# Optimization experiments

Hardware: AMD Instinct MI355X
Metric: run time of the kernel (lower is better)

## Reference

```python
import jax, jax.numpy as jnp
import numpy as np

N = 100000   # nodes
E = 1000000  # edges
F = 128      # num_features
H = 64       # hidden_size
C = 1        # num_classes
G = 128      # num graphs in batch


def gcn_conv(x, W, b, src, dst, deg_inv_sqrt):
    # PyG GCNConv: add self-loops, symmetric normalization D^-1/2 (A+I) D^-1/2, then X W + b
    h = x @ W                                   # [N, H]
    norm = deg_inv_sqrt[src] * deg_inv_sqrt[dst]  # [E]
    msg = h[src] * norm[:, None]                # gather + scale, [E, H]
    out = jnp.zeros_like(h).at[dst].add(msg)    # scatter-add to targets
    out = out + h * (deg_inv_sqrt ** 2)[:, None]  # self-loop contribution
    return out + b


def setup_inputs() -> dict:
    key = jax.random.key(0)
    ks = jax.random.split(key, 12)
    x = jax.random.normal(ks[0], (N, F), dtype=jnp.float32)
    edge_index = jax.random.randint(ks[1], (2, E), 0, N, dtype=jnp.int32).astype(jnp.int64)
    batch = jnp.sort(jax.random.randint(ks[2], (N,), 0, G, dtype=jnp.int32)).astype(jnp.int64)
    def glorot(k, fan_in, fan_out):
        s = np.float32(np.sqrt(6.0 / (fan_in + fan_out)))
        return jax.random.uniform(k, (fan_in, fan_out), jnp.float32, -s, s)
    return {
        "x": x, "edge_index": edge_index, "batch": batch,
        "W1": glorot(ks[3], F, H), "b1": jnp.zeros((H,), jnp.float32),
        "W2": glorot(ks[4], H, H), "b2": jnp.zeros((H,), jnp.float32),
        "Wl1": glorot(ks[5], H, H), "bl1": jnp.zeros((H,), jnp.float32),
        "Wl2": glorot(ks[6], H, C), "bl2": jnp.zeros((C,), jnp.float32),
    }


def reference(x, edge_index, batch, W1, b1, W2, b2, Wl1, bl1, Wl2, bl2):
    src, dst = edge_index[0], edge_index[1]
    # degree with self-loops: 1 + in-degree(target)
    deg = jnp.ones((N,), x.dtype).at[dst].add(jnp.ones((E,), x.dtype))
    deg_inv_sqrt = jax.lax.rsqrt(deg)
    h = jax.nn.relu(gcn_conv(x, W1, b1, src, dst, deg_inv_sqrt))
    h = jax.nn.relu(gcn_conv(h, W2, b2, src, dst, deg_inv_sqrt))
    g = jax.ops.segment_sum(h, batch, num_segments=G)  # global_add_pool, [G, H]
    g = jax.nn.relu(g @ Wl1 + bl1)
    out = g @ Wl2 + bl2                                # [G, 1]
    return out.squeeze(axis=1)                         # [G]
```

## Files before the change

### kernel.cpp

```cpp
#include <hip/hip_runtime.h>

#define NN 100000
#define EE 1000000
#define FF 128
#define HH 64
#define GG 128
#define NB 391
#define MMB 1563

__global__ void k_hist(const int* __restrict__ ei, int* __restrict__ cnt) {
    int e = blockIdx.x * 256 + threadIdx.x;
    if (e < EE) atomicAdd(&cnt[ei[EE + e]], 1);
}

__global__ void k_scan1(const int* __restrict__ cnt, int* __restrict__ part,
                        float* __restrict__ dis) {
    int i = blockIdx.x * 256 + threadIdx.x;
    int c = (i < NN) ? cnt[i] : 0;
    if (i < NN) dis[i] = rsqrtf((float)(c + 1));
    int v = (i < NN) ? c : 0;
    for (int o = 1; o < 64; o <<= 1) v += __shfl_xor(v, o);
    __shared__ int ws[4];
    if ((threadIdx.x & 63) == 0) ws[threadIdx.x >> 6] = v;
    __syncthreads();
    if (threadIdx.x == 0) part[blockIdx.x] = ws[0] + ws[1] + ws[2] + ws[3];
}

__global__ void k_scan2(int* __restrict__ part) {
    __shared__ int buf[512];
    int t = threadIdx.x;
    int v = (t < NB) ? part[t] : 0;
    buf[t] = v; __syncthreads();
    for (int o = 1; o < 512; o <<= 1) {
        int u = (t >= o) ? buf[t - o] : 0;
        __syncthreads();
        buf[t] += u;
        __syncthreads();
    }
    if (t < NB) part[t] = buf[t] - v;
}

__global__ void k_scan3(const int* __restrict__ cnt, const int* __restrict__ part,
                        int* __restrict__ row_ptr, int* __restrict__ cursor) {
    int i = blockIdx.x * 256 + threadIdx.x;
    int v = (i < NN) ? cnt[i] : 0;
    int lane = threadIdx.x & 63, w = threadIdx.x >> 6;
    int incl = v;
    for (int o = 1; o < 64; o <<= 1) { int u = __shfl_up(incl, o); if (lane >= o) incl += u; }
    __shared__ int ws[4];
    if (lane == 63) ws[w] = incl;
    __syncthreads();
    int woff = 0;
    for (int k = 0; k < w; ++k) woff += ws[k];
    int excl = incl - v + woff + part[blockIdx.x];
    if (i < NN) {
        row_ptr[i] = excl;
        cursor[i]  = excl;
    }
    if (i == 0) row_ptr[NN] = EE;
}

template<int K>
__device__ __forceinline__ void
mm_body(const float* __restrict__ X, const float* __restrict__ W,
        const float* __restrict__ dis, unsigned* __restrict__ Y8,
        float* __restrict__ S, float* __restrict__ Wl, int bid) {
    for (int i = threadIdx.x; i < K * HH; i += 256) Wl[i] = W[i];
    __syncthreads();
    const int lane = threadIdx.x & 63;
    const int wv   = threadIdx.x >> 6;
    const int c4   = (lane & 15) * 4;
    const int rsg  = lane >> 4;
    const int r0   = bid * 64 + wv * 16 + rsg * 4;

    const float* xr0; const float* xr1; const float* xr2; const float* xr3;
    {
        int a = r0,     b_ = r0 + 1, c = r0 + 2, d = r0 + 3;
        if (a > NN - 1) a = NN - 1;
        if (b_ > NN - 1) b_ = NN - 1;
        if (c > NN - 1) c = NN - 1;
        if (d > NN - 1) d = NN - 1;
        xr0 = X + (size_t)a * K; xr1 = X + (size_t)b_ * K;
        xr2 = X + (size_t)c * K; xr3 = X + (size_t)d * K;
    }
    float4 acc0 = {0,0,0,0}, acc1 = {0,0,0,0}, acc2 = {0,0,0,0}, acc3 = {0,0,0,0};

#pragma unroll 8
    for (int k4 = 0; k4 < K / 4; ++k4) {
        const float4 x0 = *(const float4*)(xr0 + k4 * 4);
        const float4 x1 = *(const float4*)(xr1 + k4 * 4);
        const float4 x2 = *(const float4*)(xr2 + k4 * 4);
        const float4 x3 = *(const float4*)(xr3 + k4 * 4);
        const float4 w0 = *(const float4*)&Wl[(k4 * 4 + 0) * HH + c4];
        const float4 w1 = *(const float4*)&Wl[(k4 * 4 + 1) * HH + c4];
        const float4 w2 = *(const float4*)&Wl[(k4 * 4 + 2) * HH + c4];
        const float4 w3 = *(const float4*)&Wl[(k4 * 4 + 3) * HH + c4];
#define FMA4(A, XS) \
        A.x = fmaf(XS.x, w0.x, A.x); A.y = fmaf(XS.x, w0.y, A.y); \
        A.z = fmaf(XS.x, w0.z, A.z); A.w = fmaf(XS.x, w0.w, A.w); \
        A.x = fmaf(XS.y, w1.x, A.x); A.y = fmaf(XS.y, w1.y, A.y); \
        A.z = fmaf(XS.y, w1.z, A.z); A.w = fmaf(XS.y, w1.w, A.w); \
        A.x = fmaf(XS.z, w2.x, A.x); A.y = fmaf(XS.z, w2.y, A.y); \
        A.z = fmaf(XS.z, w2.z, A.z); A.w = fmaf(XS.z, w2.w, A.w); \
        A.x = fmaf(XS.w, w3.x, A.x); A.y = fmaf(XS.w, w3.y, A.y); \
        A.z = fmaf(XS.w, w3.z, A.z); A.w = fmaf(XS.w, w3.w, A.w);
        FMA4(acc0, x0) FMA4(acc1, x1) FMA4(acc2, x2) FMA4(acc3, x3)
#undef FMA4
    }
#define STORE(I, A) { \
        const int r = r0 + I; \
        if (r < NN) { \
            const float d = dis[r]; \
            const float ax = A.x * d, ay = A.y * d, az = A.z * d, aw = A.w * d; \
            float m = fmaxf(fmaxf(fabsf(ax), fabsf(ay)), fmaxf(fabsf(az), fabsf(aw))); \
            m = fmaxf(m, __shfl_xor(m, 1)); m = fmaxf(m, __shfl_xor(m, 2)); \
            m = fmaxf(m, __shfl_xor(m, 4)); m = fmaxf(m, __shfl_xor(m, 8)); \
            const float inv = 127.0f / m; \
            int q0 = __float2int_rn(ax * inv), q1 = __float2int_rn(ay * inv); \
            int q2 = __float2int_rn(az * inv), q3 = __float2int_rn(aw * inv); \
            if (m == 0.0f) { q0 = q1 = q2 = q3 = 0; } \
            const unsigned pk = (q0 & 0xff) | ((q1 & 0xff) << 8) | \
                                ((q2 & 0xff) << 16) | ((q3 & 0xff) << 24); \
            Y8[(size_t)r * 16 + (c4 >> 2)] = pk; \
            if (c4 == 0) S[r] = m * (1.0f / 127.0f); \
        } }
    STORE(0, acc0) STORE(1, acc1) STORE(2, acc2) STORE(3, acc3)
#undef STORE
}

template<int K>
__global__ __launch_bounds__(256) void
k_matmul_b(const float* __restrict__ X, const float* __restrict__ W,
           const float* __restrict__ dis, unsigned* __restrict__ Y8,
           float* __restrict__ S) {
    __shared__ float Wl[K * HH];
    mm_body<K>(X, W, dis, Y8, S, Wl, blockIdx.x);
}

__global__ __launch_bounds__(256) void
k_mm1_place(const float* __restrict__ X, const float* __restrict__ W,
            const float* __restrict__ dis, unsigned* __restrict__ Y8,
            float* __restrict__ S, const int* __restrict__ ei,
            int* __restrict__ cursor, int* __restrict__ srcs) {
    __shared__ float Wl[FF * HH];
    if (blockIdx.x < MMB) {
        mm_body<FF>(X, W, dis, Y8, S, Wl, blockIdx.x);
    } else {
        int e = (blockIdx.x - MMB) * 256 + threadIdx.x;
        if (e < EE) {
            int d = ei[EE + e];
            int p = atomicAdd(&cursor[d], 1);
            srcs[p] = ei[e];
        }
    }
}

template<bool POOL>
__global__ __launch_bounds__(256) void
k_gconv(const int* __restrict__ row_ptr, const int* __restrict__ srcs,
        const float* __restrict__ dis, const unsigned* __restrict__ H8,
        const float* __restrict__ S, const float* __restrict__ b,
        float* __restrict__ Out, const int* __restrict__ batch,
        float* __restrict__ g) {
    const int node = blockIdx.x * 4 + (threadIdx.x >> 6);
    const int lane = threadIdx.x & 63;
    const int li   = lane & 15;
    const int qr   = lane >> 4;
    const int p0   = row_ptr[node];
    const int deg  = row_ptr[node + 1] - p0;
    const int items  = deg + 1;
    const int nbatch = (items + 7) >> 3;

    float ac0 = 0.f, ac1 = 0.f, ac2 = 0.f, ac3 = 0.f;

#define IDX(bi, dA, dB) { \
        const int iA = 8 * (bi) + qr, iB = iA + 4; \
        dA = srcs[p0 + (iA < deg ? iA : 0)]; \
        dB = srcs[p0 + (iB < deg ? iB : 0)]; }
#define VAL(bi, sA, sB, vA, vB, gA, gB) { \
        const int iA = 8 * (bi) + qr, iB = iA + 4; \
        const int rA = (iA < deg) ? sA : node; \
        const int rB = (iB < deg) ? sB : node; \
        vA = H8[(size_t)rA * 16 + li];  gA = S[rA]; \
        vB = H8[(size_t)rB * 16 + li];  gB = S[rB]; }
#define CONSUME(bi, vA, vB, gA, gB) { \
        const int iA = 8 * (bi) + qr, iB = iA + 4; \
        const float s0 = (iA <= deg) ? gA : 0.f; \
        const float s1 = (iB <= deg) ? gB : 0.f; \
        ac0 = fmaf(s0, (float)(signed char)(vA      ), ac0); \
        ac1 = fmaf(s0, (float)(signed char)(vA >> 8 ), ac1); \
        ac2 = fmaf(s0, (float)(signed char)(vA >> 16), ac2); \
        ac3 = fmaf(s0, (float)(signed char)(vA >> 24), ac3); \
        ac0 = fmaf(s1, (float)(signed char)(vB      ), ac0); \
        ac1 = fmaf(s1, (float)(signed char)(vB >> 8 ), ac1); \
        ac2 = fmaf(s1, (float)(signed char)(vB >> 16), ac2); \
        ac3 = fmaf(s1, (float)(signed char)(vB >> 24), ac3); }

    int sA0, sA1, sB0, sB1;
    unsigned vA0, vA1;
    float gA0, gA1;
    IDX(0, sA0, sA1);
    VAL(0, sA0, sA1, vA0, vA1, gA0, gA1);
    IDX(1, sB0, sB1);
    for (int bi = 1; bi < nbatch; ++bi) {
        unsigned vB0, vB1;
        float gB0, gB1;
        VAL(bi, sB0, sB1, vB0, vB1, gB0, gB1);
        IDX(bi + 1, sB0, sB1);
        CONSUME(bi - 1, vA0, vA1, gA0, gA1);
        vA0 = vB0; vA1 = vB1; gA0 = gB0; gA1 = gB1;
    }
    CONSUME(nbatch - 1, vA0, vA1, gA0, gA1);
#undef IDX
#undef VAL
#undef CONSUME

    ac0 += __shfl_xor(ac0, 16); ac0 += __shfl_xor(ac0, 32);
    ac1 += __shfl_xor(ac1, 16); ac1 += __shfl_xor(ac1, 32);
    ac2 += __shfl_xor(ac2, 16); ac2 += __shfl_xor(ac2, 32);
    ac3 += __shfl_xor(ac3, 16); ac3 += __shfl_xor(ac3, 32);
    const float c0 = __shfl(ac0, lane >> 2);
    const float c1 = __shfl(ac1, lane >> 2);
    const float c2 = __shfl(ac2, lane >> 2);
    const float c3 = __shfl(ac3, lane >> 2);
    const int m = lane & 3;
    float acc = (m == 0) ? c0 : (m == 1) ? c1 : (m == 2) ? c2 : c3;

    const float dd = dis[node];
    float v = acc * dd + b[lane];
    v = fmaxf(v, 0.0f);
    if (POOL) {
        unsafeAtomicAdd(&g[(size_t)batch[node] * HH + lane], v);
    } else {
        Out[(size_t)node * HH + lane] = v;
    }
}

__global__ void k_head1(const float* __restrict__ g, const float* __restrict__ W,
                        const float* __restrict__ b, float* __restrict__ g2) {
    const int idx = blockIdx.x * 256 + threadIdx.x;
    const int row = idx >> 6;
    const int col = idx & 63;
    const float* gr = g + (size_t)row * HH;
    float acc = b[col];
#pragma unroll
    for (int k = 0; k < HH; ++k) acc = fmaf(gr[k], W[k * HH + col], acc);
    g2[idx] = acc > 0.0f ? acc : 0.0f;
}

__global__ void k_head2(const float* __restrict__ g2, const float* __restrict__ W,
                        const float* __restrict__ b, float* __restrict__ out) {
    const int r = threadIdx.x;
    if (r >= GG) return;
    const float* gr = g2 + (size_t)r * HH;
    float acc = 0.0f;
#pragma unroll
    for (int k = 0; k < HH; ++k) acc = fmaf(gr[k], W[k], acc);
    out[r] = acc + b[0];
}

extern "C" void kernel_launch(void* const* d_in, const int* in_sizes, int n_in,
                              void* d_out, int out_size, void* d_ws, size_t ws_size,
                              hipStream_t stream) {
    const float* x   = (const float*)d_in[0];
    const int*   ei  = (const int*)d_in[1];
    const int*   bat = (const int*)d_in[2];
    const float* W1  = (const float*)d_in[3];
    const float* b1  = (const float*)d_in[4];
    const float* W2  = (const float*)d_in[5];
    const float* b2  = (const float*)d_in[6];
    const float* Wl1 = (const float*)d_in[7];
    const float* bl1 = (const float*)d_in[8];
    const float* Wl2 = (const float*)d_in[9];
    const float* bl2 = (const float*)d_in[10];
    float* out = (float*)d_out;

    char* w = (char*)d_ws;
    float*    dis     = (float*)(w);
    int*      cnt     = (int*)  (w + 400128);
    int*      row_ptr = (int*)  (w + 800256);
    int*      cursor  = (int*)  (w + 1200640);
    int*      part    = (int*)  (w + 1600768);
    int*      srcs    = (int*)  (w + 1602816);
    float*    S       = (float*)(w + 5602816);
    unsigned* H8      = (unsigned*)(w + 6002944);
    float*    A       = (float*)(w + 12402944);
    float*    g       = (float*)(w + 38002944);
    float*    g2      = g + GG * HH;

    hipMemsetAsync(cnt, 0, (size_t)NN * sizeof(int), stream);
    k_hist <<<(EE + 255) / 256, 256, 0, stream>>>(ei, cnt);
    k_scan1<<<NB, 256, 0, stream>>>(cnt, part, dis);
    k_scan2<<<1, 512, 0, stream>>>(part);
    k_scan3<<<NB, 256, 0, stream>>>(cnt, part, row_ptr, cursor);

    k_mm1_place<<<MMB + (EE + 255) / 256, 256, 0, stream>>>(x, W1, dis, H8, S, ei, cursor, srcs);
    k_gconv<false><<<NN / 4, 256, 0, stream>>>(row_ptr, srcs, dis, H8, S, b1, A, nullptr, nullptr);

    k_matmul_b<HH><<<(NN + 63) / 64, 256, 0, stream>>>(A, W2, dis, H8, S);
    hipMemsetAsync(g, 0, (size_t)GG * HH * sizeof(float), stream);
    k_gconv<true><<<NN / 4, 256, 0, stream>>>(row_ptr, srcs, dis, H8, S, b2, nullptr, bat, g);

    k_head1<<<(GG * HH) / 256, 256, 0, stream>>>(g, Wl1, bl1, g2);
    k_head2<<<1, 128, 0, stream>>>(g2, Wl2, bl2, out);
}
```

Baseline: 292.4 us.

## Replace gather aggregation with source-side push into per-edge message buffers

```diff
diff --git a/kernel.cpp b/kernel.cpp
--- a/kernel.cpp
+++ b/kernel.cpp
@@ -7,18 +7,36 @@
 #define GG 128
 #define NB 391
 #define MMB 1563
-
-__global__ void k_hist(const int* __restrict__ ei, int* __restrict__ cnt) {
+#define NQ 4
+#define QN 25000
+#define QCAP 260000
+
+__device__ inline unsigned short f2bf(float f) {
+    unsigned u = __float_as_uint(f);
+    u += 0x7fffu + ((u >> 16) & 1u);
+    return (unsigned short)(u >> 16);
+}
+__device__ inline float bf2f(unsigned short h) {
+    return __uint_as_float((unsigned)h << 16);
+}
+
+__global__ void k_hist2(const int* __restrict__ ei, int* __restrict__ cnt,
+                        int* __restrict__ cnt2) {
     int e = blockIdx.x * 256 + threadIdx.x;
-    if (e < EE) atomicAdd(&cnt[ei[EE + e]], 1);
-}
-
-__global__ void k_scan1(const int* __restrict__ cnt, int* __restrict__ part,
-                        float* __restrict__ dis) {
-    int i = blockIdx.x * 256 + threadIdx.x;
-    int c = (i < NN) ? cnt[i] : 0;
-    if (i < NN) dis[i] = rsqrtf((float)(c + 1));
-    int v = (i < NN) ? c : 0;
+    if (e < EE) {
+        atomicAdd(&cnt[ei[EE + e]], 1);
+        atomicAdd(&cnt2[ei[e]], 1);
+    }
+}
+
+__global__ void k_scan1(const int* __restrict__ cnt, const int* __restrict__ cnt2,
+                        int* __restrict__ part, float* __restrict__ dis) {
+    const int half = (blockIdx.x >= NB) ? 1 : 0;
+    const int bid  = blockIdx.x - half * NB;
+    const int i = bid * 256 + threadIdx.x;
+    const int* c = half ? cnt2 : cnt;
+    int v = (i < NN) ? c[i] : 0;
+    if (!half && i < NN) dis[i] = rsqrtf((float)(v + 1));
     for (int o = 1; o < 64; o <<= 1) v += __shfl_xor(v, o);
     __shared__ int ws[4];
     if ((threadIdx.x & 63) == 0) ws[threadIdx.x >> 6] = v;
@@ -27,24 +45,33 @@
 }
 
 __global__ void k_scan2(int* __restrict__ part) {
-    __shared__ int buf[512];
-    int t = threadIdx.x;
-    int v = (t < NB) ? part[t] : 0;
+    __shared__ int buf[1024];
+    const int t = threadIdx.x;
+    const int h = t >> 9;
+    const int j = t & 511;
+    int v = (j < NB) ? part[h * NB + j] : 0;
     buf[t] = v; __syncthreads();
     for (int o = 1; o < 512; o <<= 1) {
-        int u = (t >= o) ? buf[t - o] : 0;
+        int u = (j >= o) ? buf[t - o] : 0;
         __syncthreads();
         buf[t] += u;
         __syncthreads();
     }
-    if (t < NB) part[t] = buf[t] - v;
-}
-
-__global__ void k_scan3(const int* __restrict__ cnt, const int* __restrict__ part,
-                        int* __restrict__ row_ptr, int* __restrict__ cursor) {
-    int i = blockIdx.x * 256 + threadIdx.x;
-    int v = (i < NN) ? cnt[i] : 0;
-    int lane = threadIdx.x & 63, w = threadIdx.x >> 6;
+    if (j < NB) part[h * NB + j] = buf[t] - v;
+}
+
+__global__ void k_scan3(const int* __restrict__ cnt, const int* __restrict__ cnt2,
+                        const int* __restrict__ part,
+                        int* __restrict__ row_ptr, int* __restrict__ row_ptr2,
+                        int* __restrict__ cursor, int* __restrict__ cursor2) {
+    const int half = (blockIdx.x >= NB) ? 1 : 0;
+    const int bid  = blockIdx.x - half * NB;
+    const int i = bid * 256 + threadIdx.x;
+    const int* c  = half ? cnt2 : cnt;
+    int* rp  = half ? row_ptr2 : row_ptr;
+    int* cur = half ? cursor2 : cursor;
+    int v = (i < NN) ? c[i] : 0;
+    const int lane = threadIdx.x & 63, w = threadIdx.x >> 6;
     int incl = v;
     for (int o = 1; o < 64; o <<= 1) { int u = __shfl_up(incl, o); if (lane >= o) incl += u; }
     __shared__ int ws[4];
@@ -52,17 +79,14 @@
     __syncthreads();
     int woff = 0;
     for (int k = 0; k < w; ++k) woff += ws[k];
-    int excl = incl - v + woff + part[blockIdx.x];
-    if (i < NN) {
-        row_ptr[i] = excl;
-        cursor[i]  = excl;
-    }
-    if (i == 0) row_ptr[NN] = EE;
-}
-
-template<int K>
+    const int excl = incl - v + woff + part[blockIdx.x];
+    if (i < NN) { rp[i] = excl; cur[i] = excl; }
+    if (i == 0) rp[NN] = EE;
+}
+
+template<int K, int XBF>
 __device__ __forceinline__ void
-mm_body(const float* __restrict__ X, const float* __restrict__ W,
+mm_body(const void* __restrict__ Xv, const float* __restrict__ W,
         const float* __restrict__ dis, unsigned* __restrict__ Y8,
         float* __restrict__ S, float* __restrict__ Wl, int bid) {
     for (int i = threadIdx.x; i < K * HH; i += 256) Wl[i] = W[i];
@@ -73,24 +97,38 @@
     const int rsg  = lane >> 4;
     const int r0   = bid * 64 + wv * 16 + rsg * 4;
 
-    const float* xr0; const float* xr1; const float* xr2; const float* xr3;
+    const char* Xb = (const char*)Xv;
+    const size_t rb = (size_t)K * (XBF ? 2 : 4);
+    const char* xr0; const char* xr1; const char* xr2; const char* xr3;
     {
-        int a = r0,     b_ = r0 + 1, c = r0 + 2, d = r0 + 3;
+        int a = r0, b_ = r0 + 1, c = r0 + 2, d = r0 + 3;
         if (a > NN - 1) a = NN - 1;
         if (b_ > NN - 1) b_ = NN - 1;
         if (c > NN - 1) c = NN - 1;
         if (d > NN - 1) d = NN - 1;
-        xr0 = X + (size_t)a * K; xr1 = X + (size_t)b_ * K;
-        xr2 = X + (size_t)c * K; xr3 = X + (size_t)d * K;
+        xr0 = Xb + (size_t)a * rb; xr1 = Xb + (size_t)b_ * rb;
+        xr2 = Xb + (size_t)c * rb; xr3 = Xb + (size_t)d * rb;
     }
     float4 acc0 = {0,0,0,0}, acc1 = {0,0,0,0}, acc2 = {0,0,0,0}, acc3 = {0,0,0,0};
 
 #pragma unroll 8
     for (int k4 = 0; k4 < K / 4; ++k4) {
-        const float4 x0 = *(const float4*)(xr0 + k4 * 4);
-        const float4 x1 = *(const float4*)(xr1 + k4 * 4);
-        const float4 x2 = *(const float4*)(xr2 + k4 * 4);
-        const float4 x3 = *(const float4*)(xr3 + k4 * 4);
+        float4 x0, x1, x2, x3;
+        if (XBF) {
+            ushort4 u0 = *(const ushort4*)(xr0 + k4 * 8);
+            ushort4 u1 = *(const ushort4*)(xr1 + k4 * 8);
+            ushort4 u2 = *(const ushort4*)(xr2 + k4 * 8);
+            ushort4 u3 = *(const ushort4*)(xr3 + k4 * 8);
+            x0 = {bf2f(u0.x), bf2f(u0.y), bf2f(u0.z), bf2f(u0.w)};
+            x1 = {bf2f(u1.x), bf2f(u1.y), bf2f(u1.z), bf2f(u1.w)};
+            x2 = {bf2f(u2.x), bf2f(u2.y), bf2f(u2.z), bf2f(u2.w)};
+            x3 = {bf2f(u3.x), bf2f(u3.y), bf2f(u3.z), bf2f(u3.w)};
+        } else {
+            x0 = *(const float4*)(xr0 + k4 * 16);
+            x1 = *(const float4*)(xr1 + k4 * 16);
+            x2 = *(const float4*)(xr2 + k4 * 16);
+            x3 = *(const float4*)(xr3 + k4 * 16);
+        }
         const float4 w0 = *(const float4*)&Wl[(k4 * 4 + 0) * HH + c4];
         const float4 w1 = *(const float4*)&Wl[(k4 * 4 + 1) * HH + c4];
         const float4 w2 = *(const float4*)&Wl[(k4 * 4 + 2) * HH + c4];
@@ -128,93 +166,92 @@
 #undef STORE
 }
 
-template<int K>
+template<int K, int XBF>
 __global__ __launch_bounds__(256) void
-k_matmul_b(const float* __restrict__ X, const float* __restrict__ W,
+k_matmul_b(const void* __restrict__ X, const float* __restrict__ W,
            const float* __restrict__ dis, unsigned* __restrict__ Y8,
            float* __restrict__ S) {
     __shared__ float Wl[K * HH];
-    mm_body<K>(X, W, dis, Y8, S, Wl, blockIdx.x);
+    mm_body<K, XBF>(X, W, dis, Y8, S, Wl, blockIdx.x);
 }
 
 __global__ __launch_bounds__(256) void
 k_mm1_place(const float* __restrict__ X, const float* __restrict__ W,
             const float* __restrict__ dis, unsigned* __restrict__ Y8,
             float* __restrict__ S, const int* __restrict__ ei,
-            int* __restrict__ cursor, int* __restrict__ srcs) {
+            int* __restrict__ cursor, int* __restrict__ cursor2,
+            int* __restrict__ csc_pos) {
     __shared__ float Wl[FF * HH];
     if (blockIdx.x < MMB) {
-        mm_body<FF>(X, W, dis, Y8, S, Wl, blockIdx.x);
+        mm_body<FF, 0>(X, W, dis, Y8, S, Wl, blockIdx.x);
     } else {
         int e = (blockIdx.x - MMB) * 256 + threadIdx.x;
         if (e < EE) {
-            int d = ei[EE + e];
-            int p = atomicAdd(&cursor[d], 1);
-            srcs[p] = ei[e];
+            const int s = ei[e], d = ei[EE + e];
+            const int p = atomicAdd(&cursor[d], 1);
+            const int q = atomicAdd(&cursor2[s], 1);
+            csc_pos[q] = p;
+        }
+    }
+}
+
+__global__ __launch_bounds__(256) void
+k_scatA(const int* __restrict__ row_ptr2, const int* __restrict__ csc_pos,
+        const unsigned* __restrict__ H8, const float* __restrict__ S,
+        const int* __restrict__ row_ptr, int n0, int n1,
+        unsigned* __restrict__ msg, float* __restrict__ msgS) {
+    const int node = blockIdx.x * 16 + (threadIdx.x >> 4);
+    const int li   = threadIdx.x & 15;
+    const int tbase = (threadIdx.x & 63) & ~15;
+    const unsigned rv = H8[(size_t)node * 16 + li];
+    const float sv = S[node];
+    const int q0 = row_ptr2[node], q1 = row_ptr2[node + 1];
+    const int PB0 = row_ptr[n0], PB1 = row_ptr[n1];
+    for (int base = q0; base < q1; base += 16) {
+        const int myp = (base + li < q1) ? csc_pos[base + li] : -1;
+        const int cnt = min(16, q1 - base);
+        for (int j = 0; j < cnt; ++j) {
+            const int p = __shfl(myp, tbase + j);
+            if (p >= PB0 && p < PB1) {
+                msg[(size_t)(p - PB0) * 16 + li] = rv;
+                if (li == 0) msgS[p - PB0] = sv;
+            }
         }
     }
 }
 
 template<bool POOL>
 __global__ __launch_bounds__(256) void
-k_gconv(const int* __restrict__ row_ptr, const int* __restrict__ srcs,
-        const float* __restrict__ dis, const unsigned* __restrict__ H8,
-        const float* __restrict__ S, const float* __restrict__ b,
-        float* __restrict__ Out, const int* __restrict__ batch,
-        float* __restrict__ g) {
-    const int node = blockIdx.x * 4 + (threadIdx.x >> 6);
+k_gconvB(const int* __restrict__ row_ptr, const float* __restrict__ dis,
+         const unsigned* __restrict__ H8, const float* __restrict__ S,
+         const unsigned* __restrict__ msg, const float* __restrict__ msgS,
+         const float* __restrict__ b, int n0,
+         unsigned short* __restrict__ A, const int* __restrict__ batch,
+         float* __restrict__ g) {
+    const int node = n0 + blockIdx.x * 4 + (threadIdx.x >> 6);
     const int lane = threadIdx.x & 63;
-    const int li   = lane & 15;
-    const int qr   = lane >> 4;
-    const int p0   = row_ptr[node];
-    const int deg  = row_ptr[node + 1] - p0;
-    const int items  = deg + 1;
-    const int nbatch = (items + 7) >> 3;
-
+    const int li = lane & 15, qr = lane >> 4;
+    const int PB0 = row_ptr[n0];
+    const int p0  = row_ptr[node] - PB0;
+    const int deg = row_ptr[node + 1] - PB0 - p0;
     float ac0 = 0.f, ac1 = 0.f, ac2 = 0.f, ac3 = 0.f;
-
-#define IDX(bi, dA, dB) { \
-        const int iA = 8 * (bi) + qr, iB = iA + 4; \
-        dA = srcs[p0 + (iA < deg ? iA : 0)]; \
-        dB = srcs[p0 + (iB < deg ? iB : 0)]; }
-#define VAL(bi, sA, sB, vA, vB, gA, gB) { \
-        const int iA = 8 * (bi) + qr, iB = iA + 4; \
-        const int rA = (iA < deg) ? sA : node; \
-        const int rB = (iB < deg) ? sB : node; \
-        vA = H8[(size_t)rA * 16 + li];  gA = S[rA]; \
-        vB = H8[(size_t)rB * 16 + li];  gB = S[rB]; }
-#define CONSUME(bi, vA, vB, gA, gB) { \
-        const int iA = 8 * (bi) + qr, iB = iA + 4; \
-        const float s0 = (iA <= deg) ? gA : 0.f; \
-        const float s1 = (iB <= deg) ? gB : 0.f; \
-        ac0 = fmaf(s0, (float)(signed char)(vA      ), ac0); \
-        ac1 = fmaf(s0, (float)(signed char)(vA >> 8 ), ac1); \
-        ac2 = fmaf(s0, (float)(signed char)(vA >> 16), ac2); \
-        ac3 = fmaf(s0, (float)(signed char)(vA >> 24), ac3); \
-        ac0 = fmaf(s1, (float)(signed char)(vB      ), ac0); \
-        ac1 = fmaf(s1, (float)(signed char)(vB >> 8 ), ac1); \
-        ac2 = fmaf(s1, (float)(signed char)(vB >> 16), ac2); \
-        ac3 = fmaf(s1, (float)(signed char)(vB >> 24), ac3); }
-
-    int sA0, sA1, sB0, sB1;
-    unsigned vA0, vA1;
-    float gA0, gA1;
-    IDX(0, sA0, sA1);
-    VAL(0, sA0, sA1, vA0, vA1, gA0, gA1);
-    IDX(1, sB0, sB1);
-    for (int bi = 1; bi < nbatch; ++bi) {
-        unsigned vB0, vB1;
-        float gB0, gB1;
-        VAL(bi, sB0, sB1, vB0, vB1, gB0, gB1);
-        IDX(bi + 1, sB0, sB1);
-        CONSUME(bi - 1, vA0, vA1, gA0, gA1);
-        vA0 = vB0; vA1 = vB1; gA0 = gB0; gA1 = gB1;
-    }
-    CONSUME(nbatch - 1, vA0, vA1, gA0, gA1);
-#undef IDX
-#undef VAL
-#undef CONSUME
-
+    if (qr == 0) {
+        const unsigned v = H8[(size_t)node * 16 + li];
+        const float s = S[node];
+        ac0 = s * (float)(signed char)(v);
+        ac1 = s * (float)(signed char)(v >> 8);
+        ac2 = s * (float)(signed char)(v >> 16);
+        ac3 = s * (float)(signed char)(v >> 24);
+    }
+#pragma unroll 2
+    for (int i = qr; i < deg; i += 4) {
+        const unsigned v = msg[(size_t)(p0 + i) * 16 + li];
+        const float s = msgS[p0 + i];
+        ac0 = fmaf(s, (float)(signed char)(v), ac0);
+        ac1 = fmaf(s, (float)(signed char)(v >> 8), ac1);
+        ac2 = fmaf(s, (float)(signed char)(v >> 16), ac2);
+        ac3 = fmaf(s, (float)(signed char)(v >> 24), ac3);
+    }
     ac0 += __shfl_xor(ac0, 16); ac0 += __shfl_xor(ac0, 32);
     ac1 += __shfl_xor(ac1, 16); ac1 += __shfl_xor(ac1, 32);
     ac2 += __shfl_xor(ac2, 16); ac2 += __shfl_xor(ac2, 32);
@@ -224,7 +261,7 @@
     const float c2 = __shfl(ac2, lane >> 2);
     const float c3 = __shfl(ac3, lane >> 2);
     const int m = lane & 3;
-    float acc = (m == 0) ? c0 : (m == 1) ? c1 : (m == 2) ? c2 : c3;
+    const float acc = (m == 0) ? c0 : (m == 1) ? c1 : (m == 2) ? c2 : c3;
 
     const float dd = dis[node];
     float v = acc * dd + b[lane];
@@ -232,7 +269,7 @@
     if (POOL) {
         unsafeAtomicAdd(&g[(size_t)batch[node] * HH + lane], v);
     } else {
-        Out[(size_t)node * HH + lane] = v;
+        A[(size_t)node * HH + lane] = f2bf(v);
     }
 }
 
@@ -276,30 +313,46 @@
     float* out = (float*)d_out;
 
     char* w = (char*)d_ws;
-    float*    dis     = (float*)(w);
-    int*      cnt     = (int*)  (w + 400128);
-    int*      row_ptr = (int*)  (w + 800256);
-    int*      cursor  = (int*)  (w + 1200640);
-    int*      part    = (int*)  (w + 1600768);
-    int*      srcs    = (int*)  (w + 1602816);
-    float*    S       = (float*)(w + 5602816);
-    unsigned* H8      = (unsigned*)(w + 6002944);
-    float*    A       = (float*)(w + 12402944);
-    float*    g       = (float*)(w + 38002944);
-    float*    g2      = g + GG * HH;
-
-    hipMemsetAsync(cnt, 0, (size_t)NN * sizeof(int), stream);
-    k_hist <<<(EE + 255) / 256, 256, 0, stream>>>(ei, cnt);
-    k_scan1<<<NB, 256, 0, stream>>>(cnt, part, dis);
-    k_scan2<<<1, 512, 0, stream>>>(part);
-    k_scan3<<<NB, 256, 0, stream>>>(cnt, part, row_ptr, cursor);
-
-    k_mm1_place<<<MMB + (EE + 255) / 256, 256, 0, stream>>>(x, W1, dis, H8, S, ei, cursor, srcs);
-    k_gconv<false><<<NN / 4, 256, 0, stream>>>(row_ptr, srcs, dis, H8, S, b1, A, nullptr, nullptr);
-
-    k_matmul_b<HH><<<(NN + 63) / 64, 256, 0, stream>>>(A, W2, dis, H8, S);
+    float*    dis      = (float*)(w);
+    int*      cnt      = (int*)  (w + 400128);
+    int*      cnt2     = (int*)  (w + 800256);
+    int*      row_ptr  = (int*)  (w + 1200384);
+    int*      row_ptr2 = (int*)  (w + 1600768);
+    int*      cursor   = (int*)  (w + 2001152);
+    int*      cursor2  = (int*)  (w + 2401280);
+    int*      part     = (int*)  (w + 2801408);
+    int*      csc_pos  = (int*)  (w + 2809600);
+    float*    S        = (float*)(w + 6809600);
+    unsigned* H8       = (unsigned*)(w + 7209728);
+    float*    msgS     = (float*)(w + 13609728);
+    unsigned* msg      = (unsigned*)(w + 14649728);
+    unsigned short* A  = (unsigned short*)(w + 31289728);
+    float*    g        = (float*)(w + 44089728);
+    float*    g2       = g + GG * HH;
+
+    hipMemsetAsync(cnt, 0, 800256, stream);
+    k_hist2<<<(EE + 255) / 256, 256, 0, stream>>>(ei, cnt, cnt2);
+    k_scan1<<<2 * NB, 256, 0, stream>>>(cnt, cnt2, part, dis);
+    k_scan2<<<1, 1024, 0, stream>>>(part);
+    k_scan3<<<2 * NB, 256, 0, stream>>>(cnt, cnt2, part, row_ptr, row_ptr2, cursor, cursor2);
+
+    k_mm1_place<<<MMB + (EE + 255) / 256, 256, 0, stream>>>(
+        x, W1, dis, H8, S, ei, cursor, cursor2, csc_pos);
+    for (int k = 0; k < NQ; ++k) {
+        k_scatA<<<NN / 16, 256, 0, stream>>>(row_ptr2, csc_pos, H8, S, row_ptr,
+                                             k * QN, (k + 1) * QN, msg, msgS);
+        k_gconvB<false><<<QN / 4, 256, 0, stream>>>(row_ptr, dis, H8, S, msg, msgS,
+                                                    b1, k * QN, A, nullptr, nullptr);
+    }
+
+    k_matmul_b<HH, 1><<<MMB, 256, 0, stream>>>(A, W2, dis, H8, S);
     hipMemsetAsync(g, 0, (size_t)GG * HH * sizeof(float), stream);
-    k_gconv<true><<<NN / 4, 256, 0, stream>>>(row_ptr, srcs, dis, H8, S, b2, nullptr, bat, g);
+    for (int k = 0; k < NQ; ++k) {
+        k_scatA<<<NN / 16, 256, 0, stream>>>(row_ptr2, csc_pos, H8, S, row_ptr,
+                                             k * QN, (k + 1) * QN, msg, msgS);
+        k_gconvB<true><<<QN / 4, 256, 0, stream>>>(row_ptr, dis, H8, S, msg, msgS,
+                                                   b2, k * QN, nullptr, bat, g);
+    }
 
     k_head1<<<(GG * HH) / 256, 256, 0, stream>>>(g, Wl1, bl1, g2);
     k_head2<<<1, 128, 0, stream>>>(g2, Wl2, bl2, out);
```

After: 601.7 us. 2.06x slower.

## Embed per-row bf16 scale into int8 LSBs, drop separate scale array gathers

Applied to the files above, without the earlier changes.

```diff
diff --git a/kernel.cpp b/kernel.cpp
--- a/kernel.cpp
+++ b/kernel.cpp
@@ -7,6 +7,12 @@
 #define GG 128
 #define NB 391
 #define MMB 1563
+
+__device__ inline unsigned short f2bf(float f) {
+    unsigned u = __float_as_uint(f);
+    u += 0x7fffu + ((u >> 16) & 1u);
+    return (unsigned short)(u >> 16);
+}
 
 __global__ void k_hist(const int* __restrict__ ei, int* __restrict__ cnt) {
     int e = blockIdx.x * 256 + threadIdx.x;
@@ -64,7 +70,7 @@
 __device__ __forceinline__ void
 mm_body(const float* __restrict__ X, const float* __restrict__ W,
         const float* __restrict__ dis, unsigned* __restrict__ Y8,
-        float* __restrict__ S, float* __restrict__ Wl, int bid) {
+        float* __restrict__ Wl, int bid) {
     for (int i = threadIdx.x; i < K * HH; i += 256) Wl[i] = W[i];
     __syncthreads();
     const int lane = threadIdx.x & 63;
@@ -75,7 +81,7 @@
 
     const float* xr0; const float* xr1; const float* xr2; const float* xr3;
     {
-        int a = r0,     b_ = r0 + 1, c = r0 + 2, d = r0 + 3;
+        int a = r0, b_ = r0 + 1, c = r0 + 2, d = r0 + 3;
         if (a > NN - 1) a = NN - 1;
         if (b_ > NN - 1) b_ = NN - 1;
         if (c > NN - 1) c = NN - 1;
@@ -119,10 +125,11 @@
             int q0 = __float2int_rn(ax * inv), q1 = __float2int_rn(ay * inv); \
             int q2 = __float2int_rn(az * inv), q3 = __float2int_rn(aw * inv); \
             if (m == 0.0f) { q0 = q1 = q2 = q3 = 0; } \
-            const unsigned pk = (q0 & 0xff) | ((q1 & 0xff) << 8) | \
+            const unsigned short sb = f2bf(m * (1.0f / 127.0f)); \
+            const unsigned bit = (sb >> (c4 >> 2)) & 1u; \
+            const unsigned pk = ((q0 & 0xfe) | bit) | ((q1 & 0xff) << 8) | \
                                 ((q2 & 0xff) << 16) | ((q3 & 0xff) << 24); \
             Y8[(size_t)r * 16 + (c4 >> 2)] = pk; \
-            if (c4 == 0) S[r] = m * (1.0f / 127.0f); \
         } }
     STORE(0, acc0) STORE(1, acc1) STORE(2, acc2) STORE(3, acc3)
 #undef STORE
@@ -131,20 +138,19 @@
 template<int K>
 __global__ __launch_bounds__(256) void
 k_matmul_b(const float* __restrict__ X, const float* __restrict__ W,
-           const float* __restrict__ dis, unsigned* __restrict__ Y8,
-           float* __restrict__ S) {
+           const float* __restrict__ dis, unsigned* __restrict__ Y8) {
     __shared__ float Wl[K * HH];
-    mm_body<K>(X, W, dis, Y8, S, Wl, blockIdx.x);
+    mm_body<K>(X, W, dis, Y8, Wl, blockIdx.x);
 }
 
 __global__ __launch_bounds__(256) void
 k_mm1_place(const float* __restrict__ X, const float* __restrict__ W,
             const float* __restrict__ dis, unsigned* __restrict__ Y8,
-            float* __restrict__ S, const int* __restrict__ ei,
-            int* __restrict__ cursor, int* __restrict__ srcs) {
+            const int* __restrict__ ei, int* __restrict__ cursor,
+            int* __restrict__ srcs) {
     __shared__ float Wl[FF * HH];
     if (blockIdx.x < MMB) {
-        mm_body<FF>(X, W, dis, Y8, S, Wl, blockIdx.x);
+        mm_body<FF>(X, W, dis, Y8, Wl, blockIdx.x);
     } else {
         int e = (blockIdx.x - MMB) * 256 + threadIdx.x;
         if (e < EE) {
@@ -159,9 +165,8 @@
 __global__ __launch_bounds__(256) void
 k_gconv(const int* __restrict__ row_ptr, const int* __restrict__ srcs,
         const float* __restrict__ dis, const unsigned* __restrict__ H8,
-        const float* __restrict__ S, const float* __restrict__ b,
-        float* __restrict__ Out, const int* __restrict__ batch,
-        float* __restrict__ g) {
+        const float* __restrict__ b, float* __restrict__ Out,
+        const int* __restrict__ batch, float* __restrict__ g) {
     const int node = blockIdx.x * 4 + (threadIdx.x >> 6);
     const int lane = threadIdx.x & 63;
     const int li   = lane & 15;
@@ -177,40 +182,42 @@
         const int iA = 8 * (bi) + qr, iB = iA + 4; \
         dA = srcs[p0 + (iA < deg ? iA : 0)]; \
         dB = srcs[p0 + (iB < deg ? iB : 0)]; }
-#define VAL(bi, sA, sB, vA, vB, gA, gB) { \
+#define VAL(bi, sA, sB, vA, vB) { \
         const int iA = 8 * (bi) + qr, iB = iA + 4; \
         const int rA = (iA < deg) ? sA : node; \
         const int rB = (iB < deg) ? sB : node; \
-        vA = H8[(size_t)rA * 16 + li];  gA = S[rA]; \
-        vB = H8[(size_t)rB * 16 + li];  gB = S[rB]; }
-#define CONSUME(bi, vA, vB, gA, gB) { \
+        vA = H8[(size_t)rA * 16 + li]; \
+        vB = H8[(size_t)rB * 16 + li]; }
+#define CONSUME(bi, vA, vB) { \
         const int iA = 8 * (bi) + qr, iB = iA + 4; \
-        const float s0 = (iA <= deg) ? gA : 0.f; \
-        const float s1 = (iB <= deg) ? gB : 0.f; \
-        ac0 = fmaf(s0, (float)(signed char)(vA      ), ac0); \
+        const unsigned long long MA = __ballot((vA & 1u) != 0u); \
+        const unsigned long long MB = __ballot((vB & 1u) != 0u); \
+        float s0 = __uint_as_float(((unsigned)((MA >> (qr * 16)) & 0xffffull)) << 16); \
+        float s1 = __uint_as_float(((unsigned)((MB >> (qr * 16)) & 0xffffull)) << 16); \
+        s0 = (iA <= deg) ? s0 : 0.f; \
+        s1 = (iB <= deg) ? s1 : 0.f; \
+        ac0 = fmaf(s0, (float)(signed char)(vA & 0xfeu), ac0); \
         ac1 = fmaf(s0, (float)(signed char)(vA >> 8 ), ac1); \
         ac2 = fmaf(s0, (float)(signed char)(vA >> 16), ac2); \
         ac3 = fmaf(s0, (float)(signed char)(vA >> 24), ac3); \
-        ac0 = fmaf(s1, (float)(signed char)(vB      ), ac0); \
+        ac0 = fmaf(s1, (float)(signed char)(vB & 0xfeu), ac0); \
         ac1 = fmaf(s1, (float)(signed char)(vB >> 8 ), ac1); \
         ac2 = fmaf(s1, (float)(signed char)(vB >> 16), ac2); \
         ac3 = fmaf(s1, (float)(signed char)(vB >> 24), ac3); }
 
     int sA0, sA1, sB0, sB1;
     unsigned vA0, vA1;
-    float gA0, gA1;
     IDX(0, sA0, sA1);
-    VAL(0, sA0, sA1, vA0, vA1, gA0, gA1);
+    VAL(0, sA0, sA1, vA0, vA1);
     IDX(1, sB0, sB1);
     for (int bi = 1; bi < nbatch; ++bi) {
         unsigned vB0, vB1;
-        float gB0, gB1;
-        VAL(bi, sB0, sB1, vB0, vB1, gB0, gB1);
+        VAL(bi, sB0, sB1, vB0, vB1);
         IDX(bi + 1, sB0, sB1);
-        CONSUME(bi - 1, vA0, vA1, gA0, gA1);
-        vA0 = vB0; vA1 = vB1; gA0 = gB0; gA1 = gB1;
-    }
-    CONSUME(nbatch - 1, vA0, vA1, gA0, gA1);
+        CONSUME(bi - 1, vA0, vA1);
+        vA0 = vB0; vA1 = vB1;
+    }
+    CONSUME(nbatch - 1, vA0, vA1);
 #undef IDX
 #undef VAL
 #undef CONSUME
@@ -282,10 +289,9 @@
     int*      cursor  = (int*)  (w + 1200640);
     int*      part    = (int*)  (w + 1600768);
     int*      srcs    = (int*)  (w + 1602816);
-    float*    S       = (float*)(w + 5602816);
-    unsigned* H8      = (unsigned*)(w + 6002944);
-    float*    A       = (float*)(w + 12402944);
-    float*    g       = (float*)(w + 38002944);
+    unsigned* H8      = (unsigned*)(w + 5602816);
+    float*    A       = (float*)(w + 12002816);
+    float*    g       = (float*)(w + 37602816);
     float*    g2      = g + GG * HH;
 
     hipMemsetAsync(cnt, 0, (size_t)NN * sizeof(int), stream);
@@ -294,12 +300,12 @@
     k_scan2<<<1, 512, 0, stream>>>(part);
     k_scan3<<<NB, 256, 0, stream>>>(cnt, part, row_ptr, cursor);
 
-    k_mm1_place<<<MMB + (EE + 255) / 256, 256, 0, stream>>>(x, W1, dis, H8, S, ei, cursor, srcs);
-    k_gconv<false><<<NN / 4, 256, 0, stream>>>(row_ptr, srcs, dis, H8, S, b1, A, nullptr, nullptr);
-
-    k_matmul_b<HH><<<(NN + 63) / 64, 256, 0, stream>>>(A, W2, dis, H8, S);
+    k_mm1_place<<<MMB + (EE + 255) / 256, 256, 0, stream>>>(x, W1, dis, H8, ei, cursor, srcs);
+    k_gconv<false><<<NN / 4, 256, 0, stream>>>(row_ptr, srcs, dis, H8, b1, A, nullptr, nullptr);
+
+    k_matmul_b<HH><<<(NN + 63) / 64, 256, 0, stream>>>(A, W2, dis, H8);
     hipMemsetAsync(g, 0, (size_t)GG * HH * sizeof(float), stream);
-    k_gconv<true><<<NN / 4, 256, 0, stream>>>(row_ptr, srcs, dis, H8, S, b2, nullptr, bat, g);
+    k_gconv<true><<<NN / 4, 256, 0, stream>>>(row_ptr, srcs, dis, H8, b2, nullptr, bat, g);
 
     k_head1<<<(GG * HH) / 256, 256, 0, stream>>>(g, Wl1, bl1, g2);
     k_head2<<<1, 128, 0, stream>>>(g2, Wl2, bl2, out);
```

After: 299.9 us. 2.6% more time.

## Store layer-1 activations as bf16 and make gconv grid-stride persistent

Applied to the files above, without the earlier changes.

```diff
diff --git a/kernel.cpp b/kernel.cpp
--- a/kernel.cpp
+++ b/kernel.cpp
@@ -7,6 +7,16 @@
 #define GG 128
 #define NB 391
 #define MMB 1563
+#define GCB 2048
+
+__device__ inline unsigned short f2bf(float f) {
+    unsigned u = __float_as_uint(f);
+    u += 0x7fffu + ((u >> 16) & 1u);
+    return (unsigned short)(u >> 16);
+}
+__device__ inline float bf2f(unsigned short h) {
+    return __uint_as_float((unsigned)h << 16);
+}
 
 __global__ void k_hist(const int* __restrict__ ei, int* __restrict__ cnt) {
     int e = blockIdx.x * 256 + threadIdx.x;
@@ -60,9 +70,9 @@
     if (i == 0) row_ptr[NN] = EE;
 }
 
-template<int K>
+template<int K, int XBF>
 __device__ __forceinline__ void
-mm_body(const float* __restrict__ X, const float* __restrict__ W,
+mm_body(const void* __restrict__ Xv, const float* __restrict__ W,
         const float* __restrict__ dis, unsigned* __restrict__ Y8,
         float* __restrict__ S, float* __restrict__ Wl, int bid) {
     for (int i = threadIdx.x; i < K * HH; i += 256) Wl[i] = W[i];
@@ -73,24 +83,38 @@
     const int rsg  = lane >> 4;
     const int r0   = bid * 64 + wv * 16 + rsg * 4;
 
-    const float* xr0; const float* xr1; const float* xr2; const float* xr3;
+    const char* Xb = (const char*)Xv;
+    const size_t rb = (size_t)K * (XBF ? 2 : 4);
+    const char* xr0; const char* xr1; const char* xr2; const char* xr3;
     {
-        int a = r0,     b_ = r0 + 1, c = r0 + 2, d = r0 + 3;
+        int a = r0, b_ = r0 + 1, c = r0 + 2, d = r0 + 3;
         if (a > NN - 1) a = NN - 1;
         if (b_ > NN - 1) b_ = NN - 1;
         if (c > NN - 1) c = NN - 1;
         if (d > NN - 1) d = NN - 1;
-        xr0 = X + (size_t)a * K; xr1 = X + (size_t)b_ * K;
-        xr2 = X + (size_t)c * K; xr3 = X + (size_t)d * K;
+        xr0 = Xb + (size_t)a * rb; xr1 = Xb + (size_t)b_ * rb;
+        xr2 = Xb + (size_t)c * rb; xr3 = Xb + (size_t)d * rb;
     }
     float4 acc0 = {0,0,0,0}, acc1 = {0,0,0,0}, acc2 = {0,0,0,0}, acc3 = {0,0,0,0};
 
 #pragma unroll 8
     for (int k4 = 0; k4 < K / 4; ++k4) {
-        const float4 x0 = *(const float4*)(xr0 + k4 * 4);
-        const float4 x1 = *(const float4*)(xr1 + k4 * 4);
-        const float4 x2 = *(const float4*)(xr2 + k4 * 4);
-        const float4 x3 = *(const float4*)(xr3 + k4 * 4);
+        float4 x0, x1, x2, x3;
+        if (XBF) {
+            ushort4 u0 = *(const ushort4*)(xr0 + k4 * 8);
+            ushort4 u1 = *(const ushort4*)(xr1 + k4 * 8);
+            ushort4 u2 = *(const ushort4*)(xr2 + k4 * 8);
+            ushort4 u3 = *(const ushort4*)(xr3 + k4 * 8);
+            x0 = {bf2f(u0.x), bf2f(u0.y), bf2f(u0.z), bf2f(u0.w)};
+            x1 = {bf2f(u1.x), bf2f(u1.y), bf2f(u1.z), bf2f(u1.w)};
+            x2 = {bf2f(u2.x), bf2f(u2.y), bf2f(u2.z), bf2f(u2.w)};
+            x3 = {bf2f(u3.x), bf2f(u3.y), bf2f(u3.z), bf2f(u3.w)};
+        } else {
+            x0 = *(const float4*)(xr0 + k4 * 16);
+            x1 = *(const float4*)(xr1 + k4 * 16);
+            x2 = *(const float4*)(xr2 + k4 * 16);
+            x3 = *(const float4*)(xr3 + k4 * 16);
+        }
         const float4 w0 = *(const float4*)&Wl[(k4 * 4 + 0) * HH + c4];
         const float4 w1 = *(const float4*)&Wl[(k4 * 4 + 1) * HH + c4];
         const float4 w2 = *(const float4*)&Wl[(k4 * 4 + 2) * HH + c4];
@@ -128,13 +152,13 @@
 #undef STORE
 }
 
-template<int K>
+template<int K, int XBF>
 __global__ __launch_bounds__(256) void
-k_matmul_b(const float* __restrict__ X, const float* __restrict__ W,
+k_matmul_b(const void* __restrict__ X, const float* __restrict__ W,
            const float* __restrict__ dis, unsigned* __restrict__ Y8,
            float* __restrict__ S) {
     __shared__ float Wl[K * HH];
-    mm_body<K>(X, W, dis, Y8, S, Wl, blockIdx.x);
+    mm_body<K, XBF>(X, W, dis, Y8, S, Wl, blockIdx.x);
 }
 
 __global__ __launch_bounds__(256) void
@@ -144,7 +168,7 @@
             int* __restrict__ cursor, int* __restrict__ srcs) {
     __shared__ float Wl[FF * HH];
     if (blockIdx.x < MMB) {
-        mm_body<FF>(X, W, dis, Y8, S, Wl, blockIdx.x);
+        mm_body<FF, 0>(X, W, dis, Y8, S, Wl, blockIdx.x);
     } else {
         int e = (blockIdx.x - MMB) * 256 + threadIdx.x;
         if (e < EE) {
@@ -160,23 +184,24 @@
 k_gconv(const int* __restrict__ row_ptr, const int* __restrict__ srcs,
         const float* __restrict__ dis, const unsigned* __restrict__ H8,
         const float* __restrict__ S, const float* __restrict__ b,
-        float* __restrict__ Out, const int* __restrict__ batch,
+        unsigned short* __restrict__ Out, const int* __restrict__ batch,
         float* __restrict__ g) {
-    const int node = blockIdx.x * 4 + (threadIdx.x >> 6);
     const int lane = threadIdx.x & 63;
     const int li   = lane & 15;
     const int qr   = lane >> 4;
-    const int p0   = row_ptr[node];
-    const int deg  = row_ptr[node + 1] - p0;
-    const int items  = deg + 1;
-    const int nbatch = (items + 7) >> 3;
-
-    float ac0 = 0.f, ac1 = 0.f, ac2 = 0.f, ac3 = 0.f;
+    const float bl = b[lane];
+
+    for (int node = blockIdx.x * 4 + (threadIdx.x >> 6); node < NN; node += GCB * 4) {
+        const int p0   = row_ptr[node];
+        const int deg  = row_ptr[node + 1] - p0;
+        const int nbatch = (deg + 8) >> 3;
+
+        float ac0 = 0.f, ac1 = 0.f, ac2 = 0.f, ac3 = 0.f;
 
 #define IDX(bi, dA, dB) { \
         const int iA = 8 * (bi) + qr, iB = iA + 4; \
-        dA = srcs[p0 + (iA < deg ? iA : 0)]; \
-        dB = srcs[p0 + (iB < deg ? iB : 0)]; }
+        dA = __builtin_nontemporal_load(srcs + p0 + (iA < deg ? iA : 0)); \
+        dB = __builtin_nontemporal_load(srcs + p0 + (iB < deg ? iB : 0)); }
 #define VAL(bi, sA, sB, vA, vB, gA, gB) { \
         const int iA = 8 * (bi) + qr, iB = iA + 4; \
         const int rA = (iA < deg) ? sA : node; \
@@ -196,43 +221,43 @@
         ac2 = fmaf(s1, (float)(signed char)(vB >> 16), ac2); \
         ac3 = fmaf(s1, (float)(signed char)(vB >> 24), ac3); }
 
-    int sA0, sA1, sB0, sB1;
-    unsigned vA0, vA1;
-    float gA0, gA1;
-    IDX(0, sA0, sA1);
-    VAL(0, sA0, sA1, vA0, vA1, gA0, gA1);
-    IDX(1, sB0, sB1);
-    for (int bi = 1; bi < nbatch; ++bi) {
-        unsigned vB0, vB1;
-        float gB0, gB1;
-        VAL(bi, sB0, sB1, vB0, vB1, gB0, gB1);
-        IDX(bi + 1, sB0, sB1);
-        CONSUME(bi - 1, vA0, vA1, gA0, gA1);
-        vA0 = vB0; vA1 = vB1; gA0 = gB0; gA1 = gB1;
-    }
-    CONSUME(nbatch - 1, vA0, vA1, gA0, gA1);
+        int sA0, sA1, sB0, sB1;
+        unsigned vA0, vA1;
+        float gA0, gA1;
+        IDX(0, sA0, sA1);
+        VAL(0, sA0, sA1, vA0, vA1, gA0, gA1);
+        IDX(1, sB0, sB1);
+        for (int bi = 1; bi < nbatch; ++bi) {
+            unsigned vB0, vB1;
+            float gB0, gB1;
+            VAL(bi, sB0, sB1, vB0, vB1, gB0, gB1);
+            IDX(bi + 1, sB0, sB1);
+            CONSUME(bi - 1, vA0, vA1, gA0, gA1);
+            vA0 = vB0; vA1 = vB1; gA0 = gB0; gA1 = gB1;
+        }
+        CONSUME(nbatch - 1, vA0, vA1, gA0, gA1);
 #undef IDX
 #undef VAL
 #undef CONSUME
 
-    ac0 += __shfl_xor(ac0, 16); ac0 += __shfl_xor(ac0, 32);
-    ac1 += __shfl_xor(ac1, 16); ac1 += __shfl_xor(ac1, 32);
-    ac2 += __shfl_xor(ac2, 16); ac2 += __shfl_xor(ac2, 32);
-    ac3 += __shfl_xor(ac3, 16); ac3 += __shfl_xor(ac3, 32);
-    const float c0 = __shfl(ac0, lane >> 2);
-    const float c1 = __shfl(ac1, lane >> 2);
-    const float c2 = __shfl(ac2, lane >> 2);
-    const float c3 = __shfl(ac3, lane >> 2);
-    const int m = lane & 3;
-    float acc = (m == 0) ? c0 : (m == 1) ? c1 : (m == 2) ? c2 : c3;
-
-    const float dd = dis[node];
-    float v = acc * dd + b[lane];
-    v = fmaxf(v, 0.0f);
-    if (POOL) {
-        unsafeAtomicAdd(&g[(size_t)batch[node] * HH + lane], v);
-    } else {
-        Out[(size_t)node * HH + lane] = v;
+        ac0 += __shfl_xor(ac0, 16); ac0 += __shfl_xor(ac0, 32);
+        ac1 += __shfl_xor(ac1, 16); ac1 += __shfl_xor(ac1, 32);
+        ac2 += __shfl_xor(ac2, 16); ac2 += __shfl_xor(ac2, 32);
+        ac3 += __shfl_xor(ac3, 16); ac3 += __shfl_xor(ac3, 32);
+        const float c0 = __shfl(ac0, lane >> 2);
+        const float c1 = __shfl(ac1, lane >> 2);
+        const float c2 = __shfl(ac2, lane >> 2);
+        const float c3 = __shfl(ac3, lane >> 2);
+        const int m = lane & 3;
+        const float acc = (m == 0) ? c0 : (m == 1) ? c1 : (m == 2) ? c2 : c3;
+
+        float v = acc * dis[node] + bl;
+        v = fmaxf(v, 0.0f);
+        if (POOL) {
+            unsafeAtomicAdd(&g[(size_t)batch[node] * HH + lane], v);
+        } else {
+            __builtin_nontemporal_store(f2bf(v), Out + (size_t)node * HH + lane);
+        }
     }
 }
 
@@ -284,8 +309,8 @@
     int*      srcs    = (int*)  (w + 1602816);
     float*    S       = (float*)(w + 5602816);
     unsigned* H8      = (unsigned*)(w + 6002944);
-    float*    A       = (float*)(w + 12402944);
-    float*    g       = (float*)(w + 38002944);
+    unsigned short* A = (unsigned short*)(w + 12402944);
+    float*    g       = (float*)(w + 25202944);
     float*    g2      = g + GG * HH;
 
     hipMemsetAsync(cnt, 0, (size_t)NN * sizeof(int), stream);
@@ -295,11 +320,11 @@
     k_scan3<<<NB, 256, 0, stream>>>(cnt, part, row_ptr, cursor);
 
     k_mm1_place<<<MMB + (EE + 255) / 256, 256, 0, stream>>>(x, W1, dis, H8, S, ei, cursor, srcs);
-    k_gconv<false><<<NN / 4, 256, 0, stream>>>(row_ptr, srcs, dis, H8, S, b1, A, nullptr, nullptr);
-
-    k_matmul_b<HH><<<(NN + 63) / 64, 256, 0, stream>>>(A, W2, dis, H8, S);
+    k_gconv<false><<<GCB, 256, 0, stream>>>(row_ptr, srcs, dis, H8, S, b1, A, nullptr, nullptr);
+
+    k_matmul_b<HH, 1><<<MMB, 256, 0, stream>>>(A, W2, dis, H8, S);
     hipMemsetAsync(g, 0, (size_t)GG * HH * sizeof(float), stream);
-    k_gconv<true><<<NN / 4, 256, 0, stream>>>(row_ptr, srcs, dis, H8, S, b2, nullptr, bat, g);
+    k_gconv<true><<<GCB, 256, 0, stream>>>(row_ptr, srcs, dis, H8, S, b2, nullptr, bat, g);
 
     k_head1<<<(GG * HH) / 256, 256, 0, stream>>>(g, Wl1, bl1, g2);
     k_head2<<<1, 128, 0, stream>>>(g2, Wl2, bl2, out);
```

After: 280.0 us. 4.2% less time.
